# Kernel tuning notes

Hardware: AMD Instinct MI355X
Metric: run time of the kernel (lower is better)

## Reference

```python
import jax, jax.numpy as jnp
import numpy as np

N, R, IN, OUT = 16384, 64, 128, 128


def setup_inputs() -> dict:
    key = jax.random.key(0)
    k1, k2, k3, k4 = jax.random.split(key, 4)
    x = jax.random.normal(k1, (N, IN), dtype=jnp.float32)
    relations = jax.random.randint(k2, (N, 1), 0, R, dtype=jnp.int32)
    # kaiming_uniform_(a=sqrt(5)) on [R, in, out] -> bound = 1/sqrt(fan_in); bias uses same bound
    bound = 1.0 / np.sqrt(IN)
    w = jax.random.uniform(k3, (R, IN, OUT), dtype=jnp.float32, minval=-bound, maxval=bound)
    bias = jax.random.uniform(k4, (R, OUT), dtype=jnp.float32, minval=-bound, maxval=bound)
    return {"x": x, "relations": relations, "w": w, "bias": bias}


def reference(x, relations, w, bias):
    # Faithful math of the torch module: out[i] = x[i] @ w[relations[i,0]] + bias[relations[i,0]]
    # (original computes x.matmul(w[relations]) -> [N,1,N,out] and extracts the diagonal;
    #  this is the direct per-sample grouped GEMM form.)
    rel = relations[:, 0]                       # [N]
    w_sel = jnp.take(w, rel, axis=0)            # [N, in, out]
    out = jnp.einsum('ni,nio->no', x, w_sel)    # [N, out]
    return out + jnp.take(bias, rel, axis=0)
```

## Files before the change

### kernel.cpp

```cpp
#include <hip/hip_runtime.h>

#define N_ROWS 16384
#define R_REL  64
#define IN_D   128
#define OUT_D  128
#define BM     64
#define NS     4
#define TPB_G  256

__device__ __forceinline__ float f4c(const float4& v, int i) {
  return i == 0 ? v.x : i == 1 ? v.y : i == 2 ? v.z : v.w;
}

__global__ __launch_bounds__(256, 4) void k_pre(const int* __restrict__ rel,
                                                int* __restrict__ offsets,
                                                int* __restrict__ row_idx) {
  const int r = blockIdx.x;
  const int t = threadIdx.x;
  const int wid = t >> 6, lane = t & 63;
  __shared__ int wsum[4];
  __shared__ int sbase;
  const int4* rel4 = (const int4*)rel;

  int lt = 0;
  for (int i = t; i < N_ROWS / 4; i += 256) {
    const int4 v = rel4[i];
    lt += (v.x < r) + (v.y < r) + (v.z < r) + (v.w < r);
  }
  #pragma unroll
  for (int d = 32; d >= 1; d >>= 1) lt += __shfl_down(lt, d, 64);
  if (lane == 0) wsum[wid] = lt;
  __syncthreads();
  if (t == 0) {
    const int o = wsum[0] + wsum[1] + wsum[2] + wsum[3];
    sbase = o;
    offsets[r] = o;
    if (r == R_REL - 1) offsets[R_REL] = N_ROWS;
  }
  __syncthreads();
  int base = sbase;

  for (int c = 0; c < 16; ++c) {
    const int i4 = c * 256 + t;
    const int4 v = rel4[i4];
    const int m0 = (v.x == r), m1 = (v.y == r), m2 = (v.z == r), m3 = (v.w == r);
    const int cnt_t = m0 + m1 + m2 + m3;
    int incl = cnt_t;
    #pragma unroll
    for (int d = 1; d < 64; d <<= 1) {
      const int u = __shfl_up(incl, d, 64);
      if (lane >= d) incl += u;
    }
    if (lane == 63) wsum[wid] = incl;
    __syncthreads();
    int wbase = 0;
    for (int ww = 0; ww < wid; ++ww) wbase += wsum[ww];
    int pos = base + wbase + incl - cnt_t;
    const int row0 = i4 * 4;
    if (m0) row_idx[pos++] = row0;
    if (m1) row_idx[pos++] = row0 + 1;
    if (m2) row_idx[pos++] = row0 + 2;
    if (m3) row_idx[pos++] = row0 + 3;
    base += wsum[0] + wsum[1] + wsum[2] + wsum[3];
    __syncthreads();
  }
}

__global__ __launch_bounds__(TPB_G, 4) void k_gemm(const float* __restrict__ x,
                                                   const float* __restrict__ w,
                                                   const float* __restrict__ bias,
                                                   const int* __restrict__ offsets,
                                                   const int* __restrict__ row_idx,
                                                   float* __restrict__ out) {
  __shared__ __align__(16) float xs[BM * IN_D];
  const int r = blockIdx.y;
  const int c0 = blockIdx.z * 64;
  const int beg = offsets[r];
  const int cnt = offsets[r + 1] - beg;
  if (cnt == 0) return;
  const int t = threadIdx.x;
  const int wq = __builtin_amdgcn_readfirstlane(t >> 6);
  const int lane = t & 63;
  const int cw = c0 + wq * 16;

  float bs[16];
  #pragma unroll
  for (int j = 0; j < 16; ++j) bs[j] = bias[(size_t)r * OUT_D + cw + j];

  const float* wbase = w + (size_t)r * (IN_D * OUT_D) + cw;

  for (int tile = blockIdx.x; tile * BM < cnt; tile += NS) {
    const int m0 = beg + tile * BM;
    const int rows = min(BM, cnt - tile * BM);

    {
      const int row = t & 63;
      const int q = t >> 6;
      if (row < rows) {
        const int g = row_idx[m0 + row];
        const float4* src = (const float4*)(x + (size_t)g * IN_D) + q * 8;
        float4* dst = (float4*)xs + row * 32;
        const int sw = row & 7;
        #pragma unroll
        for (int j = 0; j < 8; ++j) dst[(q * 8 + j) ^ sw] = src[j];
      }
    }
    __syncthreads();

    float acc[16];
    #pragma unroll
    for (int j = 0; j < 16; ++j) acc[j] = 0.f;

    const float4* xp = (const float4*)xs + lane * 32;
    const int sw = lane & 7;

    #pragma unroll 4
    for (int kc = 0; kc < 32; ++kc) {
      const float4 xv = xp[kc ^ sw];
      #pragma unroll
      for (int kk = 0; kk < 4; ++kk) {
        const float* wk = wbase + (size_t)(kc * 4 + kk) * OUT_D;
        const float xk = f4c(xv, kk);
        #pragma unroll
        for (int j = 0; j < 16; ++j) acc[j] = fmaf(wk[j], xk, acc[j]);
      }
    }

    if (lane < rows) {
      const int g = row_idx[m0 + lane];
      float* op = out + (size_t)g * OUT_D + cw;
      float4 o;
      o.x = acc[0] + bs[0];  o.y = acc[1] + bs[1];
      o.z = acc[2] + bs[2];  o.w = acc[3] + bs[3];
      *(float4*)(op + 0) = o;
      o.x = acc[4] + bs[4];  o.y = acc[5] + bs[5];
      o.z = acc[6] + bs[6];  o.w = acc[7] + bs[7];
      *(float4*)(op + 4) = o;
      o.x = acc[8] + bs[8];  o.y = acc[9] + bs[9];
      o.z = acc[10] + bs[10]; o.w = acc[11] + bs[11];
      *(float4*)(op + 8) = o;
      o.x = acc[12] + bs[12]; o.y = acc[13] + bs[13];
      o.z = acc[14] + bs[14]; o.w = acc[15] + bs[15];
      *(float4*)(op + 12) = o;
    }
    __syncthreads();
  }
}

extern "C" void kernel_launch(void* const* d_in, const int* in_sizes, int n_in,
                              void* d_out, int out_size, void* d_ws, size_t ws_size,
                              hipStream_t stream) {
  const float* x    = (const float*)d_in[0];
  const int*   rel  = (const int*)d_in[1];
  const float* w    = (const float*)d_in[2];
  const float* bias = (const float*)d_in[3];
  float* out = (float*)d_out;

  int* offsets = (int*)d_ws;
  int* row_idx = (int*)d_ws + 128;

  k_pre<<<R_REL, 256, 0, stream>>>(rel, offsets, row_idx);
  k_gemm<<<dim3(NS, R_REL, 2), TPB_G, 0, stream>>>(x, w, bias, offsets, row_idx, out);
}
```

Before: 106.2 us.

## Stage weight slice in LDS and use 4x4 register tiles per thread

Each block now copies its relation's 128x64 weight slice into shared memory once. Each thread computes a 4-row by 4-column output tile from LDS, replacing the earlier one-row-by-16-columns scheme that read weights directly from global memory. This is meant to raise arithmetic intensity per LDS/global load and reuse x values across columns. In exchange, shared memory doubles to 64KB per block and the occupancy hint drops to 2 blocks per CU.

```diff
diff --git a/kernel.cpp b/kernel.cpp
--- a/kernel.cpp
+++ b/kernel.cpp
@@ -66,12 +66,13 @@
   }
 }
 
-__global__ __launch_bounds__(TPB_G, 4) void k_gemm(const float* __restrict__ x,
+__global__ __launch_bounds__(TPB_G, 2) void k_gemm(const float* __restrict__ x,
                                                    const float* __restrict__ w,
                                                    const float* __restrict__ bias,
                                                    const int* __restrict__ offsets,
                                                    const int* __restrict__ row_idx,
                                                    float* __restrict__ out) {
+  __shared__ __align__(16) float ws_[IN_D * 64];
   __shared__ __align__(16) float xs[BM * IN_D];
   const int r = blockIdx.y;
   const int c0 = blockIdx.z * 64;
@@ -79,15 +80,18 @@
   const int cnt = offsets[r + 1] - beg;
   if (cnt == 0) return;
   const int t = threadIdx.x;
-  const int wq = __builtin_amdgcn_readfirstlane(t >> 6);
-  const int lane = t & 63;
-  const int cw = c0 + wq * 16;
+  const int tx = t & 15;
+  const int ty = t >> 4;
 
-  float bs[16];
-  #pragma unroll
-  for (int j = 0; j < 16; ++j) bs[j] = bias[(size_t)r * OUT_D + cw + j];
-
-  const float* wbase = w + (size_t)r * (IN_D * OUT_D) + cw;
+  {
+    const float* wr = w + (size_t)r * (IN_D * OUT_D) + c0;
+    #pragma unroll
+    for (int i = 0; i < 8; ++i) {
+      const int id = t + i * 256;
+      const int k = id >> 4, c4 = id & 15;
+      ((float4*)ws_)[k * 16 + c4] = *(const float4*)(wr + k * OUT_D + c4 * 4);
+    }
+  }
 
   for (int tile = blockIdx.x; tile * BM < cnt; tile += NS) {
     const int m0 = beg + tile * BM;
@@ -107,41 +111,50 @@
     }
     __syncthreads();
 
-    float acc[16];
+    float4 acc[4];
     #pragma unroll
-    for (int j = 0; j < 16; ++j) acc[j] = 0.f;
+    for (int j = 0; j < 4; ++j) acc[j] = make_float4(0.f, 0.f, 0.f, 0.f);
 
-    const float4* xp = (const float4*)xs + lane * 32;
-    const int sw = lane & 7;
+    const float4* wlds = (const float4*)ws_;
+    const float4* xlds = (const float4*)xs;
 
     #pragma unroll 4
     for (int kc = 0; kc < 32; ++kc) {
-      const float4 xv = xp[kc ^ sw];
+      float4 wv[4];
+      #pragma unroll
+      for (int kk = 0; kk < 4; ++kk) wv[kk] = wlds[(kc * 4 + kk) * 16 + tx];
+      float4 xv[4];
+      #pragma unroll
+      for (int j = 0; j < 4; ++j) {
+        const int rm = ty * 4 + j;
+        xv[j] = xlds[rm * 32 + (kc ^ (rm & 7))];
+      }
       #pragma unroll
       for (int kk = 0; kk < 4; ++kk) {
-        const float* wk = wbase + (size_t)(kc * 4 + kk) * OUT_D;
-        const float xk = f4c(xv, kk);
         #pragma unroll
-        for (int j = 0; j < 16; ++j) acc[j] = fmaf(wk[j], xk, acc[j]);
+        for (int j = 0; j < 4; ++j) {
+          const float a = f4c(xv[j], kk);
+          acc[j].x += a * wv[kk].x;
+          acc[j].y += a * wv[kk].y;
+          acc[j].z += a * wv[kk].z;
+          acc[j].w += a * wv[kk].w;
+        }
       }
     }
 
-    if (lane < rows) {
-      const int g = row_idx[m0 + lane];
-      float* op = out + (size_t)g * OUT_D + cw;
-      float4 o;
-      o.x = acc[0] + bs[0];  o.y = acc[1] + bs[1];
-      o.z = acc[2] + bs[2];  o.w = acc[3] + bs[3];
-      *(float4*)(op + 0) = o;
-      o.x = acc[4] + bs[4];  o.y = acc[5] + bs[5];
-      o.z = acc[6] + bs[6];  o.w = acc[7] + bs[7];
-      *(float4*)(op + 4) = o;
-      o.x = acc[8] + bs[8];  o.y = acc[9] + bs[9];
-      o.z = acc[10] + bs[10]; o.w = acc[11] + bs[11];
-      *(float4*)(op + 8) = o;
-      o.x = acc[12] + bs[12]; o.y = acc[13] + bs[13];
-      o.z = acc[14] + bs[14]; o.w = acc[15] + bs[15];
-      *(float4*)(op + 12) = o;
+    const float4 bv = *(const float4*)(bias + (size_t)r * OUT_D + c0 + tx * 4);
+    #pragma unroll
+    for (int j = 0; j < 4; ++j) {
+      const int rm = ty * 4 + j;
+      if (rm < rows) {
+        const int g = row_idx[m0 + rm];
+        float4 o;
+        o.x = acc[j].x + bv.x;
+        o.y = acc[j].y + bv.y;
+        o.z = acc[j].z + bv.z;
+        o.w = acc[j].w + bv.w;
+        *(float4*)(out + (size_t)g * OUT_D + c0 + tx * 4) = o;
+      }
     }
     __syncthreads();
   }
```

Measured after the change: 101.5 us. 1.05x faster.
